# Optimization experiments

Hardware: AMD Instinct MI355X
Metric: run time of the kernel (lower is better)

## Reference

```python
import jax, jax.numpy as jnp
import numpy as np

DIM_MSA = 256
DIM_PAIR = 128
DIM_HID = 32
EPS = 0.001
LN_EPS = 1e-5


def setup_inputs() -> dict:
    key = jax.random.key(0)
    ks = jax.random.split(key, 8)
    b, m, n = 1, 256, 384
    x = jax.random.normal(ks[0], (b, m, n, DIM_MSA), dtype=jnp.float32)
    mask = jax.random.randint(ks[1], (b, m, n), 0, 2).astype(jnp.int32)
    ln_g = jnp.ones((DIM_MSA,), jnp.float32)
    ln_b = jnp.zeros((DIM_MSA,), jnp.float32)
    s = 1.0 / np.sqrt(DIM_MSA)
    wl = jax.random.normal(ks[2], (DIM_MSA, DIM_HID), jnp.float32) * s
    bl = jnp.zeros((DIM_HID,), jnp.float32)
    wr = jax.random.normal(ks[3], (DIM_MSA, DIM_HID), jnp.float32) * s
    br = jnp.zeros((DIM_HID,), jnp.float32)
    wo = jax.random.normal(ks[4], (DIM_HID * DIM_HID, DIM_PAIR), jnp.float32) / np.sqrt(DIM_HID * DIM_HID)
    bo = jnp.zeros((DIM_PAIR,), jnp.float32)
    return {"x": x, "mask": mask, "ln_g": ln_g, "ln_b": ln_b,
            "wl": wl, "bl": bl, "wr": wr, "br": br, "wo": wo, "bo": bo}


def reference(x, mask, ln_g, ln_b, wl, bl, wr, br, wo, bo):
    # LayerNorm over last dim
    mu = jnp.mean(x, axis=-1, keepdims=True)
    var = jnp.mean(jnp.square(x - mu), axis=-1, keepdims=True)
    xn = (x - mu) * jax.lax.rsqrt(var + LN_EPS) * ln_g + ln_b
    left = xn @ wl + bl    # [b,m,n,c]
    right = xn @ wr + br   # [b,m,n,d]
    m = mask.astype(x.dtype)  # 0/1 mask [b,m,n]
    left = left * m[..., None]
    right = right * m[..., None]
    # masked outer-product sum over MSA dim m, no 6D materialization
    outer = jnp.einsum('bmic,bmjd->bijcd', left, right)
    b_, i_, j_ = outer.shape[0], outer.shape[1], outer.shape[2]
    outer = outer.reshape(b_, i_, j_, DIM_HID * DIM_HID)
    out = outer @ wo + bo  # [b,i,j,pairwise]
    cnt = jnp.einsum('bmi,bmj->bij', m, m)  # valid-pair counts
    return out / (cnt[..., None] + EPS)
```

## Files before the change

kernel.cpp:

```cpp
#include <hip/hip_runtime.h>
#include <hip/hip_bf16.h>
#include <stdint.h>


typedef float f32x4 __attribute__((ext_vector_type(4)));
typedef __bf16 bf16x8 __attribute__((ext_vector_type(8)));
typedef __bf16 bf16x4 __attribute__((ext_vector_type(4)));

#define NSEQ 384
#define NMSA 256

typedef const __attribute__((address_space(1))) unsigned int* gptr_t;
typedef __attribute__((address_space(3))) unsigned int* lptr_t;

__device__ __forceinline__ void gload_lds16(const void* g, void* l) {
    __builtin_amdgcn_global_load_lds((gptr_t)g, (lptr_t)l, 16, 0, 0);
}

__global__ __launch_bounds__(256) void prep_kernel(
    const float* __restrict__ wo, __bf16* __restrict__ woT)
{
    int gid = blockIdx.x * 256 + threadIdx.x;
    int p = gid >> 10, q = gid & 1023;
    int d = q >> 5, c = q & 31;
    woT[gid] = (__bf16)wo[(c * 32 + d) * 128 + p];
}

__global__ __launch_bounds__(256) void prep_wg_kernel(
    const float* __restrict__ wl, const float* __restrict__ wr,
    const float* __restrict__ bl, const float* __restrict__ br,
    const float* __restrict__ ln_g, const float* __restrict__ ln_b,
    __bf16* __restrict__ wg, float* __restrict__ Gc, float* __restrict__ B2)
{
    const int c = blockIdx.x;
    const int k = threadIdx.x;
    float w = (c < 32) ? wl[k * 32 + c] : wr[k * 32 + (c - 32)];
    __bf16 wgb = (__bf16)(w * ln_g[k]);
    wg[c * 256 + k] = wgb;
    float gsum = (float)wgb;
    float bsum = w * ln_b[k];
    __shared__ float sg[4], sb[4];
    for (int off = 32; off; off >>= 1) {
        gsum += __shfl_down(gsum, off);
        bsum += __shfl_down(bsum, off);
    }
    int wid = k >> 6, lane = k & 63;
    if (lane == 0) { sg[wid] = gsum; sb[wid] = bsum; }
    __syncthreads();
    if (k == 0) {
        Gc[c] = sg[0] + sg[1] + sg[2] + sg[3];
        B2[c] = sb[0] + sb[1] + sb[2] + sb[3] + ((c < 32) ? bl[c] : br[c - 32]);
    }
}

__global__ __launch_bounds__(256) void cnt_kernel(
    const int* __restrict__ mask, float* __restrict__ inv_cnt)
{
    const int i = blockIdx.x;
    const int t = threadIdx.x;
    __shared__ int mi[NMSA];
    mi[t] = mask[t * NSEQ + i];
    __syncthreads();
    for (int j = t; j < NSEQ; j += 256) {
        int acc = 0;
        for (int m = 0; m < NMSA; ++m)
            acc += mi[m] & mask[m * NSEQ + j];
        inv_cnt[i * NSEQ + j] = 1.0f / ((float)acc + 0.001f);
    }
}

__global__ __launch_bounds__(256) void ln_proj_kernel(
    const float* __restrict__ x, const int* __restrict__ mask,
    const __bf16* __restrict__ wg, const float* __restrict__ Gc,
    const float* __restrict__ B2,
    __bf16* __restrict__ leftT, __bf16* __restrict__ rightT)
{
    const int n = blockIdx.x;
    const int tid = threadIdx.x;
    __shared__ __bf16 xnT[NMSA * 40];
    __shared__ float muS[NMSA], rsS[NMSA], maskS[NMSA], GcS[64], B2S[64];

    if (tid < 64) { GcS[tid] = Gc[tid]; B2S[tid] = B2[tid]; }
    maskS[tid] = (float)mask[tid * NSEQ + n];

    const int wid = tid >> 6, lane = tid & 63;
    const int lhi = lane >> 4, llo = lane & 15;
    float ps[8] = {}, pq[8] = {};
    f32x4 acc[4][4] = {};

    for (int k0 = 0; k0 < 256; k0 += 32) {
        #pragma unroll
        for (int cc = 0; cc < 8; ++cc) {
            int ch = tid + cc * 256;
            int mR = ch >> 3, c4 = ch & 7;
            f32x4 v = *reinterpret_cast<const f32x4*>(x + ((size_t)mR * NSEQ + n) * 256 + k0 + c4 * 4);
            ps[cc] += v[0] + v[1] + v[2] + v[3];
            pq[cc] += v[0]*v[0] + v[1]*v[1] + v[2]*v[2] + v[3]*v[3];
            __bf16* dst = xnT + mR * 40 + c4 * 4;
            dst[0] = (__bf16)v[0]; dst[1] = (__bf16)v[1];
            dst[2] = (__bf16)v[2]; dst[3] = (__bf16)v[3];
        }
        __syncthreads();
        bf16x8 af[4], bfr[4];
        #pragma unroll
        for (int fr = 0; fr < 4; ++fr)
            af[fr] = *reinterpret_cast<const bf16x8*>(wg + (size_t)(fr * 16 + llo) * 256 + k0 + lhi * 8);
        #pragma unroll
        for (int fc = 0; fc < 4; ++fc)
            bfr[fc] = *reinterpret_cast<const bf16x8*>(xnT + (wid * 64 + fc * 16 + llo) * 40 + lhi * 8);
        #pragma unroll
        for (int fr = 0; fr < 4; ++fr)
            #pragma unroll
            for (int fc = 0; fc < 4; ++fc)
                acc[fr][fc] = __builtin_amdgcn_mfma_f32_16x16x32_bf16(af[fr], bfr[fc], acc[fr][fc], 0, 0, 0);
        __syncthreads();
    }

    #pragma unroll
    for (int cc = 0; cc < 8; ++cc) {
        float s = ps[cc], q = pq[cc];
        s += __shfl_xor(s, 1); q += __shfl_xor(q, 1);
        s += __shfl_xor(s, 2); q += __shfl_xor(q, 2);
        s += __shfl_xor(s, 4); q += __shfl_xor(q, 4);
        if ((tid & 7) == 0) {
            int m = (tid >> 3) + cc * 32;
            float mu = s * (1.f / 256.f);
            float var = q * (1.f / 256.f) - mu * mu;
            muS[m] = mu;
            rsS[m] = rsqrtf(var + 1e-5f);
        }
    }
    __syncthreads();

    #pragma unroll
    for (int fr = 0; fr < 4; ++fr) {
        #pragma unroll
        for (int fc = 0; fc < 4; ++fc) {
            int mR = wid * 64 + fc * 16 + llo;
            float mv = maskS[mR], rs = rsS[mR], mu = muS[mR];
            #pragma unroll
            for (int r = 0; r < 4; ++r) {
                int c = fr * 16 + lhi * 4 + r;
                float val = (acc[fr][fc][r] - mu * GcS[c]) * rs + B2S[c];
                __bf16 bv = (__bf16)(val * mv);
                if (c < 32) leftT [(size_t)(n * 32 + c)        * 256 + mR] = bv;
                else        rightT[(size_t)(n * 32 + (c - 32)) * 256 + mR] = bv;
            }
        }
    }
}

__global__ __launch_bounds__(512, 2) void outer_gemm_kernel(
    const __bf16* __restrict__ leftT, const __bf16* __restrict__ rightT,
    const __bf16* __restrict__ woT, const float* __restrict__ bo,
    const float* __restrict__ inv_cnt, float* __restrict__ out)
{
    __shared__ char smem[131072];
    const int tid = threadIdx.x;
    const int wid = tid >> 6, lane = tid & 63;
    const int lhi = lane >> 4, llo = lane & 15;
    const int wr = wid >> 2, wc = wid & 3;

    int wg_ = blockIdx.x;
    int l  = (wg_ & 7) * 288 + (wg_ >> 3);
    int bj = l / 48, bi = l % 48;

    char* Abuf[2] = { smem,         smem + 65536 };
    char* Bbuf[2] = { smem + 32768, smem + 98304 };

    auto STAGE = [&](int buf, int k0) {
        #pragma unroll
        for (int it = 0; it < 4; ++it) {
            int q = it * 512 + wid * 64 + lane;
            int r = q >> 3;
            int s = (q & 7) ^ (r & 7);
            int ldsoff = (it * 512 + wid * 64) * 16;
            gload_lds16(leftT  + (size_t)(bi * 256 + r) * 256 + k0 + s * 8, Abuf[buf] + ldsoff);
            gload_lds16(rightT + (size_t)(bj * 256 + r) * 256 + k0 + s * 8, Bbuf[buf] + ldsoff);
        }
    };

    f32x4 acc[8][4] = {};

    STAGE(0, 0);
    #pragma unroll
    for (int t = 0; t < 4; ++t) {
        if (t < 3) {
            STAGE((t + 1) & 1, (t + 1) * 64);
            asm volatile("s_waitcnt vmcnt(8)" ::: "memory");
        } else {
            asm volatile("s_waitcnt vmcnt(0)" ::: "memory");
        }
        __builtin_amdgcn_s_barrier();
        __builtin_amdgcn_sched_barrier(0);
        const __bf16* Al = (const __bf16*)Abuf[t & 1];
        const __bf16* Bl = (const __bf16*)Bbuf[t & 1];
        #pragma unroll
        for (int kk = 0; kk < 2; ++kk) {
            bf16x8 af[8], bfv[4];
            int sb = kk * 4 + lhi;
            #pragma unroll
            for (int fr = 0; fr < 8; ++fr) {
                int row = wr * 128 + fr * 16 + llo;
                af[fr] = *(const bf16x8*)(Al + row * 64 + ((sb ^ (row & 7)) << 3));
            }
            #pragma unroll
            for (int fc = 0; fc < 4; ++fc) {
                int row = wc * 64 + fc * 16 + llo;
                bfv[fc] = *(const bf16x8*)(Bl + row * 64 + ((sb ^ (row & 7)) << 3));
            }
            #pragma unroll
            for (int fr = 0; fr < 8; ++fr)
                #pragma unroll
                for (int fc = 0; fc < 4; ++fc)
                    acc[fr][fc] = __builtin_amdgcn_mfma_f32_16x16x32_bf16(af[fr], bfv[fc], acc[fr][fc], 0, 0, 0);
        }
        __builtin_amdgcn_sched_barrier(0);
        __builtin_amdgcn_s_barrier();
    }

    __bf16* Aep = (__bf16*)smem;
    #pragma unroll
    for (int fr = 0; fr < 8; ++fr) {
        #pragma unroll
        for (int fc = 0; fc < 4; ++fc) {
            int ij = (wr * 4 + (fr >> 1)) * 8 + wc * 2 + (fc >> 1);
            int half = fc & 1;
            int t = llo * 4 + (fr & 1) * 2 + (lhi >> 1);
            int tp = t ^ ((t >> 3) & 7) ^ (ij & 7);
            bf16x4 v;
            v[0] = (__bf16)acc[fr][fc][0]; v[1] = (__bf16)acc[fr][fc][1];
            v[2] = (__bf16)acc[fr][fc][2]; v[3] = (__bf16)acc[fr][fc][3];
            *(bf16x4*)(Aep + half * 32768 + ij * 512 + tp * 8 + (lhi & 1) * 4) = v;
        }
    }
    __syncthreads();

    const int kw = wid & 1, nw = wid >> 1;
    const __bf16* Asrc = Aep + kw * 32768;
    f32x4 eacc[4][2] = {};
    #pragma unroll 2
    for (int k0 = 0; k0 < 512; k0 += 32) {
        bf16x8 bw0 = *(const bf16x8*)(woT + (size_t)(nw * 32 + llo)      * 1024 + kw * 512 + k0 + lhi * 8);
        bf16x8 bw1 = *(const bf16x8*)(woT + (size_t)(nw * 32 + 16 + llo) * 1024 + kw * 512 + k0 + lhi * 8);
        int t = (k0 >> 3) + lhi;
        int txor = (t >> 3) & 7;
        #pragma unroll
        for (int mf = 0; mf < 4; ++mf) {
            int ij = mf * 16 + llo;
            int tp = t ^ txor ^ (ij & 7);
            bf16x8 a = *(const bf16x8*)(Asrc + ij * 512 + tp * 8);
            eacc[mf][0] = __builtin_amdgcn_mfma_f32_16x16x32_bf16(a, bw0, eacc[mf][0], 0, 0, 0);
            eacc[mf][1] = __builtin_amdgcn_mfma_f32_16x16x32_bf16(a, bw1, eacc[mf][1], 0, 0, 0);
        }
    }
    __syncthreads();

    float* scratch = (float*)smem;
    if (kw == 1) {
        #pragma unroll
        for (int mf = 0; mf < 4; ++mf)
            #pragma unroll
            for (int pf = 0; pf < 2; ++pf) {
                int p = nw * 32 + pf * 16 + llo;
                #pragma unroll
                for (int r = 0; r < 4; ++r)
                    scratch[(mf * 16 + lhi * 4 + r) * 132 + p] = eacc[mf][pf][r];
            }
    }
    __syncthreads();
    if (kw == 0) {
        #pragma unroll
        for (int mf = 0; mf < 4; ++mf)
            #pragma unroll
            for (int pf = 0; pf < 2; ++pf) {
                int p = nw * 32 + pf * 16 + llo;
                float bov = bo[p];
                #pragma unroll
                for (int r = 0; r < 4; ++r) {
                    int ij = mf * 16 + lhi * 4 + r;
                    int i = bi * 8 + (ij >> 3), j = bj * 8 + (ij & 7);
                    size_t idx = (size_t)i * NSEQ + j;
                    out[idx * 128 + p] = (eacc[mf][pf][r] + scratch[ij * 132 + p] + bov) * inv_cnt[idx];
                }
            }
    }
}

extern "C" void kernel_launch(void* const* d_in, const int* in_sizes, int n_in,
                              void* d_out, int out_size, void* d_ws, size_t ws_size,
                              hipStream_t stream) {
    const float* x    = (const float*)d_in[0];
    const int*   mask = (const int*)  d_in[1];
    const float* ln_g = (const float*)d_in[2];
    const float* ln_b = (const float*)d_in[3];
    const float* wl   = (const float*)d_in[4];
    const float* bl   = (const float*)d_in[5];
    const float* wr   = (const float*)d_in[6];
    const float* br   = (const float*)d_in[7];
    const float* wo   = (const float*)d_in[8];
    const float* bo   = (const float*)d_in[9];
    float* out = (float*)d_out;

    char* ws = (char*)d_ws;
    __bf16* leftT   = (__bf16*)(ws);
    __bf16* rightT  = (__bf16*)(ws + 6291456);
    __bf16* woT     = (__bf16*)(ws + 12582912);
    __bf16* wg      = (__bf16*)(ws + 12845056);
    float*  Gc      = (float*) (ws + 12877824);
    float*  B2      = (float*) (ws + 12878080);
    float*  inv_cnt = (float*) (ws + 12878336);

    prep_kernel<<<512, 256, 0, stream>>>(wo, woT);
    prep_wg_kernel<<<64, 256, 0, stream>>>(wl, wr, bl, br, ln_g, ln_b, wg, Gc, B2);
    cnt_kernel<<<NSEQ, 256, 0, stream>>>(mask, inv_cnt);
    ln_proj_kernel<<<NSEQ, 256, 0, stream>>>(x, mask, wg, Gc, B2, leftT, rightT);
    outer_gemm_kernel<<<2304, 512, 0, stream>>>(leftT, rightT, woT, bo, inv_cnt, out);
}
```

Baseline: 218.6 us.

## Shrink outer-GEMM tile to 8x4 pairs for higher occupancy and smaller LDS

The fused outer-product + projection kernel now computes an 8x4 (i,j) tile per workgroup instead of 8x8. It uses a 256x128 accumulator per block, 32-wide K steps with a smaller double buffer, and 48KB LDS instead of 128KB, with launch bounds raised to 4 blocks per CU. The epilogue projection runs in two K halves that reuse the same LDS region, which removes the cross-wave scratch reduction. In exchange, twice as many blocks re-read the left operand and woT, and there are more barriers per K step.

```diff
diff --git a/kernel.cpp b/kernel.cpp
--- a/kernel.cpp
+++ b/kernel.cpp
@@ -150,140 +150,114 @@
     }
 }
 
-__global__ __launch_bounds__(512, 2) void outer_gemm_kernel(
+__global__ __launch_bounds__(512, 4) void outer_gemm_kernel(
     const __bf16* __restrict__ leftT, const __bf16* __restrict__ rightT,
     const __bf16* __restrict__ woT, const float* __restrict__ bo,
     const float* __restrict__ inv_cnt, float* __restrict__ out)
 {
-    __shared__ char smem[131072];
+    __shared__ char smem[49152];
     const int tid = threadIdx.x;
     const int wid = tid >> 6, lane = tid & 63;
     const int lhi = lane >> 4, llo = lane & 15;
-    const int wr = wid >> 2, wc = wid & 3;
+    const int wr = wid >> 1, wc = wid & 1;
 
     int wg_ = blockIdx.x;
-    int l  = (wg_ & 7) * 288 + (wg_ >> 3);
-    int bj = l / 48, bi = l % 48;
-
-    char* Abuf[2] = { smem,         smem + 65536 };
-    char* Bbuf[2] = { smem + 32768, smem + 98304 };
-
-    auto STAGE = [&](int buf, int k0) {
-        #pragma unroll
-        for (int it = 0; it < 4; ++it) {
-            int q = it * 512 + wid * 64 + lane;
-            int r = q >> 3;
-            int s = (q & 7) ^ (r & 7);
-            int ldsoff = (it * 512 + wid * 64) * 16;
-            gload_lds16(leftT  + (size_t)(bi * 256 + r) * 256 + k0 + s * 8, Abuf[buf] + ldsoff);
-            gload_lds16(rightT + (size_t)(bj * 256 + r) * 256 + k0 + s * 8, Bbuf[buf] + ldsoff);
+    int l  = (wg_ & 7) * 576 + (wg_ >> 3);
+    int bJ = l / 48, bI = l % 48;
+
+    auto STAGE = [&](int buf, int tt) {
+        char* base = smem + buf * 24576;
+        #pragma unroll
+        for (int ph = 0; ph < 2; ++ph) {
+            int q = ph * 512 + tid;
+            int r = q >> 2;
+            int ssrc = (q & 3) ^ ((r >> 1) & 3);
+            gload_lds16(leftT + (size_t)(bI * 256 + r) * 256 + tt * 32 + ssrc * 8,
+                        base + (ph * 512 + wid * 64) * 16);
+        }
+        {
+            int r = tid >> 2;
+            int ssrc = (tid & 3) ^ ((r >> 1) & 3);
+            gload_lds16(rightT + (size_t)(bJ * 128 + r) * 256 + tt * 32 + ssrc * 8,
+                        base + 16384 + (wid * 64) * 16);
         }
     };
 
-    f32x4 acc[8][4] = {};
+    f32x4 acc[4][4] = {};
 
     STAGE(0, 0);
-    #pragma unroll
-    for (int t = 0; t < 4; ++t) {
-        if (t < 3) {
-            STAGE((t + 1) & 1, (t + 1) * 64);
-            asm volatile("s_waitcnt vmcnt(8)" ::: "memory");
-        } else {
-            asm volatile("s_waitcnt vmcnt(0)" ::: "memory");
-        }
-        __builtin_amdgcn_s_barrier();
-        __builtin_amdgcn_sched_barrier(0);
-        const __bf16* Al = (const __bf16*)Abuf[t & 1];
-        const __bf16* Bl = (const __bf16*)Bbuf[t & 1];
-        #pragma unroll
-        for (int kk = 0; kk < 2; ++kk) {
-            bf16x8 af[8], bfv[4];
-            int sb = kk * 4 + lhi;
-            #pragma unroll
-            for (int fr = 0; fr < 8; ++fr) {
-                int row = wr * 128 + fr * 16 + llo;
-                af[fr] = *(const bf16x8*)(Al + row * 64 + ((sb ^ (row & 7)) << 3));
+    __syncthreads();
+    #pragma unroll
+    for (int t = 0; t < 8; ++t) {
+        if (t < 7) STAGE((t + 1) & 1, t + 1);
+        const __bf16* Al = (const __bf16*)(smem + (t & 1) * 24576);
+        const __bf16* Bl = Al + 8192;
+        bf16x8 af[4], bfv[4];
+        #pragma unroll
+        for (int fr = 0; fr < 4; ++fr) {
+            int row = wr * 64 + fr * 16 + llo;
+            af[fr] = *(const bf16x8*)(Al + row * 32 + ((lhi ^ ((row >> 1) & 3)) << 3));
+        }
+        #pragma unroll
+        for (int fc = 0; fc < 4; ++fc) {
+            int row = wc * 64 + fc * 16 + llo;
+            bfv[fc] = *(const bf16x8*)(Bl + row * 32 + ((lhi ^ ((row >> 1) & 3)) << 3));
+        }
+        #pragma unroll
+        for (int fr = 0; fr < 4; ++fr)
+            #pragma unroll
+            for (int fc = 0; fc < 4; ++fc)
+                acc[fr][fc] = __builtin_amdgcn_mfma_f32_16x16x32_bf16(af[fr], bfv[fc], acc[fr][fc], 0, 0, 0);
+        __syncthreads();
+    }
+
+    __bf16* Aep = (__bf16*)smem;
+    f32x4 eacc[2] = {};
+    const int p = wid * 16 + llo;
+    #pragma unroll
+    for (int h = 0; h < 2; ++h) {
+        #pragma unroll
+        for (int fr = 0; fr < 4; ++fr) {
+            #pragma unroll
+            for (int fj = 0; fj < 2; ++fj) {
+                int fc = h + fj * 2;
+                int ij = (wr * 2 + (fr >> 1)) * 4 + wc * 2 + fj;
+                int tt = llo * 4 + (fr & 1) * 2 + (lhi >> 1);
+                int tp = tt ^ ((tt >> 3) & 7) ^ (ij & 7);
+                bf16x4 v;
+                v[0] = (__bf16)acc[fr][fc][0]; v[1] = (__bf16)acc[fr][fc][1];
+                v[2] = (__bf16)acc[fr][fc][2]; v[3] = (__bf16)acc[fr][fc][3];
+                *(bf16x4*)(Aep + ij * 512 + tp * 8 + (lhi & 1) * 4) = v;
             }
-            #pragma unroll
-            for (int fc = 0; fc < 4; ++fc) {
-                int row = wc * 64 + fc * 16 + llo;
-                bfv[fc] = *(const bf16x8*)(Bl + row * 64 + ((sb ^ (row & 7)) << 3));
+        }
+        __syncthreads();
+        #pragma unroll 2
+        for (int k0 = 0; k0 < 512; k0 += 32) {
+            bf16x8 bw = *(const bf16x8*)(woT + (size_t)p * 1024 + h * 512 + k0 + lhi * 8);
+            int tt = (k0 >> 3) + lhi;
+            int txor = (tt >> 3) & 7;
+            #pragma unroll
+            for (int mf = 0; mf < 2; ++mf) {
+                int ij = mf * 16 + llo;
+                int tp = tt ^ txor ^ (ij & 7);
+                bf16x8 a = *(const bf16x8*)(Aep + ij * 512 + tp * 8);
+                eacc[mf] = __builtin_amdgcn_mfma_f32_16x16x32_bf16(a, bw, eacc[mf], 0, 0, 0);
             }
-            #pragma unroll
-            for (int fr = 0; fr < 8; ++fr)
-                #pragma unroll
-                for (int fc = 0; fc < 4; ++fc)
-                    acc[fr][fc] = __builtin_amdgcn_mfma_f32_16x16x32_bf16(af[fr], bfv[fc], acc[fr][fc], 0, 0, 0);
-        }
-        __builtin_amdgcn_sched_barrier(0);
-        __builtin_amdgcn_s_barrier();
-    }
-
-    __bf16* Aep = (__bf16*)smem;
-    #pragma unroll
-    for (int fr = 0; fr < 8; ++fr) {
-        #pragma unroll
-        for (int fc = 0; fc < 4; ++fc) {
-            int ij = (wr * 4 + (fr >> 1)) * 8 + wc * 2 + (fc >> 1);
-            int half = fc & 1;
-            int t = llo * 4 + (fr & 1) * 2 + (lhi >> 1);
-            int tp = t ^ ((t >> 3) & 7) ^ (ij & 7);
-            bf16x4 v;
-            v[0] = (__bf16)acc[fr][fc][0]; v[1] = (__bf16)acc[fr][fc][1];
-            v[2] = (__bf16)acc[fr][fc][2]; v[3] = (__bf16)acc[fr][fc][3];
-            *(bf16x4*)(Aep + half * 32768 + ij * 512 + tp * 8 + (lhi & 1) * 4) = v;
-        }
-    }
-    __syncthreads();
-
-    const int kw = wid & 1, nw = wid >> 1;
-    const __bf16* Asrc = Aep + kw * 32768;
-    f32x4 eacc[4][2] = {};
-    #pragma unroll 2
-    for (int k0 = 0; k0 < 512; k0 += 32) {
-        bf16x8 bw0 = *(const bf16x8*)(woT + (size_t)(nw * 32 + llo)      * 1024 + kw * 512 + k0 + lhi * 8);
-        bf16x8 bw1 = *(const bf16x8*)(woT + (size_t)(nw * 32 + 16 + llo) * 1024 + kw * 512 + k0 + lhi * 8);
-        int t = (k0 >> 3) + lhi;
-        int txor = (t >> 3) & 7;
-        #pragma unroll
-        for (int mf = 0; mf < 4; ++mf) {
-            int ij = mf * 16 + llo;
-            int tp = t ^ txor ^ (ij & 7);
-            bf16x8 a = *(const bf16x8*)(Asrc + ij * 512 + tp * 8);
-            eacc[mf][0] = __builtin_amdgcn_mfma_f32_16x16x32_bf16(a, bw0, eacc[mf][0], 0, 0, 0);
-            eacc[mf][1] = __builtin_amdgcn_mfma_f32_16x16x32_bf16(a, bw1, eacc[mf][1], 0, 0, 0);
-        }
-    }
-    __syncthreads();
-
-    float* scratch = (float*)smem;
-    if (kw == 1) {
-        #pragma unroll
-        for (int mf = 0; mf < 4; ++mf)
-            #pragma unroll
-            for (int pf = 0; pf < 2; ++pf) {
-                int p = nw * 32 + pf * 16 + llo;
-                #pragma unroll
-                for (int r = 0; r < 4; ++r)
-                    scratch[(mf * 16 + lhi * 4 + r) * 132 + p] = eacc[mf][pf][r];
-            }
-    }
-    __syncthreads();
-    if (kw == 0) {
-        #pragma unroll
-        for (int mf = 0; mf < 4; ++mf)
-            #pragma unroll
-            for (int pf = 0; pf < 2; ++pf) {
-                int p = nw * 32 + pf * 16 + llo;
-                float bov = bo[p];
-                #pragma unroll
-                for (int r = 0; r < 4; ++r) {
-                    int ij = mf * 16 + lhi * 4 + r;
-                    int i = bi * 8 + (ij >> 3), j = bj * 8 + (ij & 7);
-                    size_t idx = (size_t)i * NSEQ + j;
-                    out[idx * 128 + p] = (eacc[mf][pf][r] + scratch[ij * 132 + p] + bov) * inv_cnt[idx];
-                }
-            }
+        }
+        if (h == 0) __syncthreads();
+    }
+
+    const float bov = bo[p];
+    #pragma unroll
+    for (int mf = 0; mf < 2; ++mf) {
+        #pragma unroll
+        for (int r = 0; r < 4; ++r) {
+            int ij = mf * 16 + lhi * 4 + r;
+            int i = bI * 8 + (ij >> 2);
+            int j = bJ * 4 + (ij & 3);
+            size_t idx = (size_t)i * NSEQ + j;
+            out[idx * 128 + p] = (eacc[mf][r] + bov) * inv_cnt[idx];
+        }
     }
 }
 
@@ -315,5 +289,5 @@
     prep_wg_kernel<<<64, 256, 0, stream>>>(wl, wr, bl, br, ln_g, ln_b, wg, Gc, B2);
     cnt_kernel<<<NSEQ, 256, 0, stream>>>(mask, inv_cnt);
     ln_proj_kernel<<<NSEQ, 256, 0, stream>>>(x, mask, wg, Gc, B2, leftT, rightT);
-    outer_gemm_kernel<<<2304, 512, 0, stream>>>(leftT, rightT, woT, bo, inv_cnt, out);
-}
+    outer_gemm_kernel<<<4608, 512, 0, stream>>>(leftT, rightT, woT, bo, inv_cnt, out);
+}
```

Result: slower. 259.7 us (+18.8%).
